# Optimization experiments

Measured on AMD Instinct MI355X. Metric: run time of the kernel, lower is better.

Reference implementation:

```python
import jax, jax.numpy as jnp
import numpy as np

EPS = 1e-8
LOSS_EPS = 1e-6
LOSS_WEIGHT = 1.0
N_BOXES = 262144

# ---------- rotated-2D-box helpers (mmcv diff_iou_rotated style) ----------

def box2corners_2d(box):
    # box: (N,5) = (x, y, w, h, alpha) -> corners (N,4,2), CCW order
    x, y, w, h, a = box[:, 0], box[:, 1], box[:, 2], box[:, 3], box[:, 4]
    x4 = jnp.array([0.5, -0.5, -0.5, 0.5], box.dtype) * w[:, None]   # (N,4)
    y4 = jnp.array([0.5, 0.5, -0.5, -0.5], box.dtype) * h[:, None]
    c, s = jnp.cos(a)[:, None], jnp.sin(a)[:, None]
    rx = x4 * c - y4 * s + x[:, None]
    ry = x4 * s + y4 * c + y[:, None]
    return jnp.stack([rx, ry], axis=-1)


def box_intersection(c1, c2):
    # segment-segment intersections between the 4 edges of each box
    # c1, c2: (N,4,2) -> pts (N,16,2), mask (N,16)
    l1 = jnp.concatenate([c1, jnp.roll(c1, -1, axis=1)], axis=-1)[:, :, None, :]  # (N,4,1,4)
    l2 = jnp.concatenate([c2, jnp.roll(c2, -1, axis=1)], axis=-1)[:, None, :, :]  # (N,1,4,4)
    x1, y1, x2, y2 = l1[..., 0], l1[..., 1], l1[..., 2], l1[..., 3]
    x3, y3, x4, y4 = l2[..., 0], l2[..., 1], l2[..., 2], l2[..., 3]
    num = (y4 - y3) * (x2 - x1) - (x4 - x3) * (y2 - y1)
    den_t = (x4 - x3) * (y1 - y3) - (y4 - y3) * (x1 - x3)
    den_u = (x2 - x1) * (y1 - y3) - (y2 - y1) * (x1 - x3)
    safe = jnp.where(num == 0.0, 1.0, num)
    t = jnp.where(num == 0.0, -1.0, den_t / safe)
    u = jnp.where(num == 0.0, -1.0, -den_u / safe)
    mask = (t > 0.0) & (t < 1.0) & (u > 0.0) & (u < 1.0)  # (N,4,4)
    t2 = den_t / (num + EPS)
    pts = jnp.stack([x1 + t2 * (x2 - x1), y1 + t2 * (y2 - y1)], axis=-1)
    pts = pts * mask[..., None]
    n = c1.shape[0]
    return pts.reshape(n, 16, 2), mask.reshape(n, 16)


def box_in_box(c1, c2):
    # which corners of box1 lie inside box2; c1,c2: (N,4,2) -> (N,4) bool
    a, b, d = c2[:, 0:1], c2[:, 1:2], c2[:, 3:4]
    ab, ad, am = b - a, d - a, c1 - a
    p_ab = jnp.sum(ab * am, -1) / jnp.sum(ab * ab, -1)
    p_ad = jnp.sum(ad * am, -1) / jnp.sum(ad * ad, -1)
    tol = 1e-6
    return (p_ab > -tol) & (p_ab < 1 + tol) & (p_ad > -tol) & (p_ad < 1 + tol)


def polygon_area(vertices, mask):
    # sort valid vertices CCW around their mean, close polygon, shoelace area
    # vertices: (N,24,2), mask: (N,24) bool -> area (N,)
    maskf = mask.astype(vertices.dtype)
    nv = jnp.maximum(jnp.sum(maskf, axis=1, keepdims=True), 1.0)
    mean = jnp.sum(vertices * maskf[..., None], axis=1, keepdims=True) / nv[..., None]
    v = vertices - mean
    ang = jnp.arctan2(v[..., 1], v[..., 0])
    # invalid vertices get huge, index-increasing keys so they sort last (stable)
    ang = jnp.where(mask, ang, 1e6 + jnp.arange(24, dtype=vertices.dtype))
    order = jnp.argsort(ang, axis=1)                         # (N,24) int
    vs = jnp.take_along_axis(v, order[..., None], axis=1)    # (N,24,2)
    ms = jnp.take_along_axis(mask, order, axis=1)
    first = vs[:, 0:1]                                       # first (valid) vertex
    vs = jnp.where(ms[..., None], vs, first)                 # pad closes polygon
    x, y = vs[..., 0], vs[..., 1]
    xn, yn = jnp.roll(x, -1, axis=1), jnp.roll(y, -1, axis=1)
    return 0.5 * jnp.abs(jnp.sum(x * yn - y * xn, axis=1))


def diff_iou_rotated_3d(b1, b2):
    # b1, b2: (N,7) = (x,y,z,w,h,l,alpha) -> IoU3D (N,)
    c1 = box2corners_2d(b1[:, jnp.array([0, 1, 3, 4, 6])])
    c2 = box2corners_2d(b2[:, jnp.array([0, 1, 3, 4, 6])])
    ipts, imask = box_intersection(c1, c2)
    m12 = box_in_box(c1, c2)
    m21 = box_in_box(c2, c1)
    vertices = jnp.concatenate([c1, c2, ipts], axis=1)   # (N,24,2)
    mask = jnp.concatenate([m12, m21, imask], axis=1)    # (N,24)
    inter_2d = polygon_area(vertices, mask)
    zmax1, zmin1 = b1[:, 2] + 0.5 * b1[:, 5], b1[:, 2] - 0.5 * b1[:, 5]
    zmax2, zmin2 = b2[:, 2] + 0.5 * b2[:, 5], b2[:, 2] - 0.5 * b2[:, 5]
    z_ov = jnp.maximum(jnp.minimum(zmax1, zmax2) - jnp.maximum(zmin1, zmin2), 0.0)
    inter_3d = inter_2d * z_ov
    vol1 = b1[:, 3] * b1[:, 4] * b1[:, 5]
    vol2 = b2[:, 3] * b2[:, 4] * b2[:, 5]
    return inter_3d / (vol1 + vol2 - inter_3d)


def corners_from_bboxes3d(b):
    # (N,7) -> (N,8,3); rotation about axis=1 (mmdet3d rotation_3d_in_axis)
    corners_norm = jnp.array([[-0.5, -0.5, -0.5], [-0.5, -0.5, 0.5],
                              [-0.5, 0.5, 0.5], [-0.5, 0.5, -0.5],
                              [0.5, -0.5, -0.5], [0.5, -0.5, 0.5],
                              [0.5, 0.5, 0.5], [0.5, 0.5, -0.5]], b.dtype)
    corners = corners_norm[None] * b[:, None, 3:6]          # (N,8,3)
    c, s = jnp.cos(b[:, 6])[:, None], jnp.sin(b[:, 6])[:, None]
    x, y, z = corners[..., 0], corners[..., 1], corners[..., 2]
    xr = x * c + z * s
    zr = -x * s + z * c
    return jnp.stack([xr, y, zr], axis=-1) + b[:, None, :3]


def diou_3d_loss(pred, target):
    iou3d = jnp.nan_to_num(diff_iou_rotated_3d(pred, target), nan=0.0)
    ctd = jnp.sum((pred[:, :3] - target[:, :3]) ** 2, axis=-1)
    cnd = jnp.mean(jnp.sum((corners_from_bboxes3d(pred)
                            - corners_from_bboxes3d(target)) ** 2, axis=-1), axis=1)
    did = jnp.sum(target[:, 3:6] ** 2, axis=-1)
    return 1.0 - iou3d + (ctd + cnd) / (ctd + cnd + did + LOSS_EPS)


def setup_inputs() -> dict:
    key = jax.random.key(0)
    k1, k2, k3, k4, k5 = jax.random.split(key, 5)
    xy = jax.random.uniform(k1, (N_BOXES, 2), minval=-40.0, maxval=40.0)
    z = jax.random.uniform(k2, (N_BOXES, 1), minval=-3.0, maxval=1.0)
    dims = jax.random.uniform(k3, (N_BOXES, 3), minval=0.8, maxval=4.0)
    ang = jax.random.uniform(k4, (N_BOXES, 1), minval=-np.pi, maxval=np.pi)
    target = jnp.concatenate([xy, z, dims, ang], axis=1).astype(jnp.float32)
    noise = jax.random.normal(k5, (N_BOXES, 7), jnp.float32) * \
        jnp.array([0.3, 0.3, 0.1, 0.2, 0.2, 0.2, 0.1], jnp.float32)
    pred = target + noise
    pred = pred.at[:, 3:6].set(jnp.maximum(pred[:, 3:6], 0.1))
    return {"pred": pred, "target": target}


def reference(pred, target):
    # DIOU3DLoss.forward with weight=None, reduction='mean'
    return LOSS_WEIGHT * jnp.mean(diou_3d_loss(pred, target))
```

## Files before the change

### kernel.cpp

```cpp
#include <hip/hip_runtime.h>
#include <math.h>

#define EPSI 1e-8f

typedef __fp16 half2v __attribute__((ext_vector_type(2)));

__device__ __forceinline__ float frcp(float x) { return __builtin_amdgcn_rcpf(x); }

#define CE(A, B) {                                  \
    unsigned ka = key[A], kb = key[B];              \
    key[A] = ka < kb ? ka : kb;                     \
    key[B] = ka < kb ? kb : ka; }

__global__ __launch_bounds__(256, 4) void diou3d_main(
    const float* __restrict__ pred, const float* __restrict__ tgt,
    float* __restrict__ partial, int n)
{
    __shared__ unsigned vbuf[24][256];
    __shared__ float wsum[4];
    int tx = threadIdx.x;
    int tid = blockIdx.x * 256 + tx;
    float loss = 0.0f;
    if (tid < n) {
        const float* P = pred + (size_t)tid * 7;
        const float* T = tgt  + (size_t)tid * 7;
        float p0 = P[0], p1 = P[1], p2 = P[2], p3 = P[3], p4 = P[4], p5 = P[5], p6 = P[6];
        float t0 = T[0], t1 = T[1], t2 = T[2], t3 = T[3], t4 = T[4], t5 = T[5], t6 = T[6];

        float sp, cp, st, ct;
        __sincosf(p6, &sp, &cp);
        __sincosf(t6, &st, &ct);
        const float hx[4] = {0.5f, -0.5f, -0.5f, 0.5f};
        const float hy[4] = {0.5f, 0.5f, -0.5f, -0.5f};
        float c1x[4], c1y[4], c2x[4], c2y[4];
#pragma unroll
        for (int k = 0; k < 4; k++) {
            float xa = hx[k] * p3, ya = hy[k] * p4;
            c1x[k] = xa * cp - ya * sp + p0;
            c1y[k] = xa * sp + ya * cp + p1;
            float xb = hx[k] * t3, yb = hy[k] * t4;
            c2x[k] = xb * ct - yb * st + t0;
            c2y[k] = xb * st + yb * ct + t1;
        }

        float vx[24], vy[24];
        float ma[24];

#pragma unroll
        for (int k = 0; k < 4; k++) {
            vx[k] = c1x[k];     vy[k] = c1y[k];
            vx[4 + k] = c2x[k]; vy[4 + k] = c2y[k];
        }

        float e1x[2], e1y[2], e2x[2], e2y[2];
        e1x[0] = c1x[1] - c1x[0]; e1y[0] = c1y[1] - c1y[0];
        e1x[1] = c1x[2] - c1x[1]; e1y[1] = c1y[2] - c1y[1];
        e2x[0] = c2x[1] - c2x[0]; e2y[0] = c2y[1] - c2y[0];
        e2x[1] = c2x[2] - c2x[1]; e2y[1] = c2y[2] - c2y[1];

        float rb[2][2];
#pragma unroll
        for (int a = 0; a < 2; a++)
#pragma unroll
            for (int b = 0; b < 2; b++) {
                float bn = e2y[b] * e1x[a] - e2x[b] * e1y[a];
                rb[a][b] = frcp(bn + EPSI);
            }

        float A_[2][4], Bv[4], C_[2][4], Dv[4];
#pragma unroll
        for (int b = 0; b < 2; b++)
#pragma unroll
            for (int i = 0; i < 4; i++)
                A_[b][i] = e2x[b] * c1y[i] - e2y[b] * c1x[i];
#pragma unroll
        for (int j = 0; j < 4; j++)
            Bv[j] = e2x[j & 1] * c2y[j] - e2y[j & 1] * c2x[j];
#pragma unroll
        for (int a = 0; a < 2; a++)
#pragma unroll
            for (int j = 0; j < 4; j++)
                C_[a][j] = e1x[a] * c2y[j] - e1y[a] * c2x[j];
#pragma unroll
        for (int i = 0; i < 4; i++)
            Dv[i] = e1x[i & 1] * c1y[i] - e1y[i & 1] * c1x[i];

        float hmn[4], hmx[4];
#pragma unroll
        for (int i = 0; i < 4; i++) {
            float gmn = 0.0f, gmx = 0.0f;
#pragma unroll
            for (int j = 0; j < 4; j++) {
                const int a = i & 1, b = j & 1;
                float g = A_[b][i] - Bv[j];
                float h = C_[a][j] - Dv[i];
                float r = rb[a][b];
                float tau = g * r;
                float ups = h * r;
                bool mt = (i < 2) ? (tau > 0.0f && tau < 1.0f)
                                  : (tau > -1.0f && tau < 0.0f);
                bool mu = (j < 2) ? (ups > 0.0f && ups < 1.0f)
                                  : (ups > -1.0f && ups < 0.0f);
                const int idx = 8 + i * 4 + j;
                vx[idx] = fmaf(tau, e1x[a], c1x[i]);
                vy[idx] = fmaf(tau, e1y[a], c1y[i]);
                ma[idx] = (mt && mu) ? 1.0f : 0.0f;
                if (j == 0) gmn = g; else if (j == 1) gmn = fminf(gmn, g);
                else if (j == 2) gmx = g; else gmx = fmaxf(gmx, g);
                if (i == 0) hmn[j] = h;
                else if (i == 1) hmn[j] = fminf(hmn[j], h);
                else if (i == 2) hmx[j] = h;
                else hmx[j] = fmaxf(hmx[j], h);
            }
            ma[i] = (gmn >= 0.0f && gmx <= 0.0f) ? 1.0f : 0.0f;
        }
#pragma unroll
        for (int j = 0; j < 4; j++)
            ma[4 + j] = (hmn[j] >= 0.0f && hmx[j] <= 0.0f) ? 1.0f : 0.0f;

        float cntf = 0.0f, sx = 0.0f, sy = 0.0f;
#pragma unroll
        for (int k = 0; k < 24; k++) {
            cntf += ma[k];
            sx = fmaf(ma[k], vx[k], sx);
            sy = fmaf(ma[k], vy[k], sy);
        }
        int ic = (int)cntf;
        float rnv = frcp(fmaxf(cntf, 1.0f));
        float mx = sx * rnv, my = sy * rnv;

        unsigned key[24];
#pragma unroll
        for (int k = 0; k < 24; k++) {
            float ux = vx[k] - mx, uy = vy[k] - my;
            half2v h = __builtin_amdgcn_cvt_pkrtz(ux, uy);
            vbuf[k][tx] = __builtin_bit_cast(unsigned, h);
            float d = fabsf(ux) + fabsf(uy);
            float pq = ux * frcp(d);
            pq = (d == 0.0f) ? 0.0f : pq;
            float ang = (uy < 0.0f) ? (pq - 1.0f) : (1.0f - pq);
            unsigned u = __float_as_uint(ang);
            u ^= (unsigned)(((int)u >> 31)) | 0x80000000u;
            unsigned kk = (u & 0xFFFFFFE0u) | (unsigned)k;
            key[k] = (ma[k] != 0.0f) ? kk : (0xFFFFFFE0u | (unsigned)k);
        }

#pragma unroll
        for (int p = 1; p < 32; p <<= 1) {
#pragma unroll
            for (int k = p; k >= 1; k >>= 1) {
#pragma unroll
                for (int j = k & (p - 1); j + k < 32; j += 2 * k) {
#pragma unroll
                    for (int i = 0; i < k; i++) {
                        int lo = i + j, hi = i + j + k;
                        if (hi < 24 && (lo / (2 * p) == hi / (2 * p))) {
                            CE(lo, hi);
                        }
                    }
                }
            }
        }

        float gx[12], gy[12];
#pragma unroll
        for (int s = 0; s < 12; s++) {
            int idx = (int)(key[s] & 31u);
            half2v h = __builtin_bit_cast(half2v, vbuf[idx][tx]);
            gx[s] = (float)h.x; gy[s] = (float)h.y;
        }

        float x0 = gx[0], y0 = gy[0];
#pragma unroll
        for (int s = 0; s < 12; s++) {
            bool v = (s < ic);
            gx[s] = v ? gx[s] : x0;
            gy[s] = v ? gy[s] : y0;
        }
        float area2 = 0.0f;
#pragma unroll
        for (int s = 0; s < 12; s++) {
            int ns = (s == 11) ? 0 : s + 1;
            area2 += gx[s] * gy[ns] - gy[s] * gx[ns];
        }
        float inter2d = 0.5f * fabsf(area2);

        float zmax1 = p2 + 0.5f * p5, zmin1 = p2 - 0.5f * p5;
        float zmax2 = t2 + 0.5f * t5, zmin2 = t2 - 0.5f * t5;
        float zov = fmaxf(fminf(zmax1, zmax2) - fmaxf(zmin1, zmin2), 0.0f);
        float inter3d = inter2d * zov;
        float vol1 = p3 * p4 * p5, vol2 = t3 * t4 * t5;
        float iou = inter3d / (vol1 + vol2 - inter3d);
        if (isnan(iou)) iou = 0.0f;

        float d0 = p0 - t0, d1 = p1 - t1, d2 = p2 - t2;
        float ctd = d0 * d0 + d1 * d1 + d2 * d2;

        float cosd = cp * ct + sp * st;
        float dp2 = p3 * p3 + p4 * p4 + p5 * p5;
        float dt2 = t3 * t3 + t4 * t4 + t5 * t5;
        float crossd = p3 * t3 * cosd + p4 * t4 + p5 * t5 * cosd;
        float cnd = ctd + 0.25f * (dp2 + dt2) - 0.5f * crossd;

        float dterm = (ctd + cnd) / (ctd + cnd + dt2 + 1e-6f);
        loss = 1.0f - iou + dterm;
    }

#pragma unroll
    for (int off = 32; off > 0; off >>= 1) loss += __shfl_down(loss, off);
    int lane = tx & 63, wid = tx >> 6;
    if (lane == 0) wsum[wid] = loss;
    __syncthreads();
    if (tx == 0)
        partial[blockIdx.x] = wsum[0] + wsum[1] + wsum[2] + wsum[3];
}

__global__ __launch_bounds__(256) void diou3d_reduce(
    const float* __restrict__ partial, int nblocks, float* __restrict__ out, float invn)
{
    float s = 0.0f;
    for (int i = threadIdx.x; i < nblocks; i += 256) s += partial[i];
#pragma unroll
    for (int off = 32; off > 0; off >>= 1) s += __shfl_down(s, off);
    __shared__ float wsum[4];
    int lane = threadIdx.x & 63, wid = threadIdx.x >> 6;
    if (lane == 0) wsum[wid] = s;
    __syncthreads();
    if (threadIdx.x == 0)
        out[0] = (wsum[0] + wsum[1] + wsum[2] + wsum[3]) * invn;
}

extern "C" void kernel_launch(void* const* d_in, const int* in_sizes, int n_in,
                              void* d_out, int out_size, void* d_ws, size_t ws_size,
                              hipStream_t stream) {
    const float* pred = (const float*)d_in[0];
    const float* tgt  = (const float*)d_in[1];
    float* out = (float*)d_out;
    int n = in_sizes[0] / 7;
    const int T = 256;
    int blocks = (n + T - 1) / T;
    float* partial = (float*)d_ws;
    diou3d_main<<<blocks, T, 0, stream>>>(pred, tgt, partial, n);
    diou3d_reduce<<<1, 256, 0, stream>>>(partial, blocks, out, 1.0f / (float)n);
}
```

Baseline: 75.16 us.

## Fuse final reduction via atomicAdd and vectorize box loads with float4

The separate single-block reduce kernel is removed. Each block now atomically adds its scaled partial sum into the output, which is zeroed with a memset beforehand. Box parameters are loaded as two overlapping float4 reads per box instead of seven scalar loads. The float4 reads from a 7-float stride are not 16-byte aligned and may become split or slower accesses. The atomic ordering also makes the float sum nondeterministic, and a memset is added to the stream.

New measurement: 79.11 us. 1.05x slower.

```diff
diff --git a/kernel.cpp b/kernel.cpp
--- a/kernel.cpp
+++ b/kernel.cpp
@@ -14,7 +14,7 @@
 
 __global__ __launch_bounds__(256, 4) void diou3d_main(
     const float* __restrict__ pred, const float* __restrict__ tgt,
-    float* __restrict__ partial, int n)
+    float* __restrict__ out, float invn, int n)
 {
     __shared__ unsigned vbuf[24][256];
     __shared__ float wsum[4];
@@ -24,8 +24,12 @@
     if (tid < n) {
         const float* P = pred + (size_t)tid * 7;
         const float* T = tgt  + (size_t)tid * 7;
-        float p0 = P[0], p1 = P[1], p2 = P[2], p3 = P[3], p4 = P[4], p5 = P[5], p6 = P[6];
-        float t0 = T[0], t1 = T[1], t2 = T[2], t3 = T[3], t4 = T[4], t5 = T[5], t6 = T[6];
+        float4 Pa = *reinterpret_cast<const float4*>(P);
+        float4 Pb = *reinterpret_cast<const float4*>(P + 3);
+        float4 Ta = *reinterpret_cast<const float4*>(T);
+        float4 Tb = *reinterpret_cast<const float4*>(T + 3);
+        float p0 = Pa.x, p1 = Pa.y, p2 = Pa.z, p3 = Pb.x, p4 = Pb.y, p5 = Pb.z, p6 = Pb.w;
+        float t0 = Ta.x, t1 = Ta.y, t2 = Ta.z, t3 = Tb.x, t4 = Tb.y, t5 = Tb.z, t6 = Tb.w;
 
         float sp, cp, st, ct;
         __sincosf(p6, &sp, &cp);
@@ -212,22 +216,7 @@
     if (lane == 0) wsum[wid] = loss;
     __syncthreads();
     if (tx == 0)
-        partial[blockIdx.x] = wsum[0] + wsum[1] + wsum[2] + wsum[3];
-}
-
-__global__ __launch_bounds__(256) void diou3d_reduce(
-    const float* __restrict__ partial, int nblocks, float* __restrict__ out, float invn)
-{
-    float s = 0.0f;
-    for (int i = threadIdx.x; i < nblocks; i += 256) s += partial[i];
-#pragma unroll
-    for (int off = 32; off > 0; off >>= 1) s += __shfl_down(s, off);
-    __shared__ float wsum[4];
-    int lane = threadIdx.x & 63, wid = threadIdx.x >> 6;
-    if (lane == 0) wsum[wid] = s;
-    __syncthreads();
-    if (threadIdx.x == 0)
-        out[0] = (wsum[0] + wsum[1] + wsum[2] + wsum[3]) * invn;
+        atomicAdd(out, (wsum[0] + wsum[1] + wsum[2] + wsum[3]) * invn);
 }
 
 extern "C" void kernel_launch(void* const* d_in, const int* in_sizes, int n_in,
@@ -239,7 +228,6 @@
     int n = in_sizes[0] / 7;
     const int T = 256;
     int blocks = (n + T - 1) / T;
-    float* partial = (float*)d_ws;
-    diou3d_main<<<blocks, T, 0, stream>>>(pred, tgt, partial, n);
-    diou3d_reduce<<<1, 256, 0, stream>>>(partial, blocks, out, 1.0f / (float)n);
+    hipMemsetAsync(out, 0, sizeof(float), stream);
+    diou3d_main<<<blocks, T, 0, stream>>>(pred, tgt, out, 1.0f / (float)n, n);
 }
```
